# Kernel optimization log

Measured on AMD Instinct MI355X. Metric: run time of the kernel, lower is better.

Reference implementation:

```python
import jax, jax.numpy as jnp
import numpy as np

N_NODES = 50000
N_EDGES = 800000
N_GRAPHS = 128
F_IN = 36
HEADS1 = 10
OUT_DIM = 128


def _gat_layer(x, src, dst, W, a_src, a_dst, b, heads, out_c):
    # x: [N, Fin]; W: [Fin, heads*out_c]; a_src/a_dst: [heads, out_c]; b: [heads*out_c]
    N = x.shape[0]
    h = (x @ W).reshape(N, heads, out_c)                      # [N,H,C]
    al_s = jnp.einsum('nhc,hc->nh', h, a_src)                 # [N,H]
    al_d = jnp.einsum('nhc,hc->nh', h, a_dst)                 # [N,H]
    e = jax.nn.leaky_relu(al_s[src] + al_d[dst], negative_slope=0.2)  # [E,H]
    # segment-softmax over incoming edges of each dst node
    m = jax.ops.segment_max(e, dst, num_segments=N)
    m = jnp.where(jnp.isfinite(m), m, 0.0)
    p = jnp.exp(e - m[dst])
    s = jax.ops.segment_sum(p, dst, num_segments=N)
    alpha = p / (s[dst] + 1e-16)                              # [E,H]
    out = jax.ops.segment_sum(alpha[:, :, None] * h[src], dst, num_segments=N)  # [N,H,C]
    return out.reshape(N, heads * out_c) + b


def setup_inputs() -> dict:
    key = jax.random.key(0)
    ks = jax.random.split(key, 12)
    x = jax.random.normal(ks[0], (N_NODES, F_IN), dtype=jnp.float32)
    edge_index = jax.random.randint(ks[1], (2, N_EDGES), 0, N_NODES, dtype=jnp.int64)
    batch = jnp.sort(jax.random.randint(ks[2], (N_NODES,), 0, N_GRAPHS, dtype=jnp.int64))
    g = 0.1  # glorot-ish scale
    W1 = jax.random.normal(ks[3], (F_IN, HEADS1 * F_IN), dtype=jnp.float32) * g
    att_src1 = jax.random.normal(ks[4], (HEADS1, F_IN), dtype=jnp.float32) * g
    att_dst1 = jax.random.normal(ks[5], (HEADS1, F_IN), dtype=jnp.float32) * g
    b1 = jnp.zeros((HEADS1 * F_IN,), dtype=jnp.float32)
    W2 = jax.random.normal(ks[6], (HEADS1 * F_IN, OUT_DIM), dtype=jnp.float32) * g
    att_src2 = jax.random.normal(ks[7], (1, OUT_DIM), dtype=jnp.float32) * g
    att_dst2 = jax.random.normal(ks[8], (1, OUT_DIM), dtype=jnp.float32) * g
    b2 = jnp.zeros((OUT_DIM,), dtype=jnp.float32)
    fc_w = jax.random.normal(ks[9], (OUT_DIM, OUT_DIM), dtype=jnp.float32) * g
    fc_b = jnp.zeros((OUT_DIM,), dtype=jnp.float32)
    return {"x": x, "edge_index": edge_index, "batch": batch,
            "W1": W1, "att_src1": att_src1, "att_dst1": att_dst1, "b1": b1,
            "W2": W2, "att_src2": att_src2, "att_dst2": att_dst2, "b2": b2,
            "fc_w": fc_w, "fc_b": fc_b}


def reference(x, edge_index, batch, W1, att_src1, att_dst1, b1,
              W2, att_src2, att_dst2, b2, fc_w, fc_b):
    N = x.shape[0]
    # PyG GATConv adds self loops by default
    loops = jnp.arange(N, dtype=edge_index.dtype)
    src = jnp.concatenate([edge_index[0], loops])
    dst = jnp.concatenate([edge_index[1], loops])
    # eval mode: dropouts are identity
    h = jax.nn.elu(_gat_layer(x, src, dst, W1, att_src1, att_dst1, b1, HEADS1, F_IN))
    h = _gat_layer(h, src, dst, W2, att_src2, att_dst2, b2, 1, OUT_DIM)
    h = jax.nn.relu(h)
    # global max pool over graphs
    g = jax.ops.segment_max(h, batch, num_segments=N_GRAPHS)
    g = jnp.where(jnp.isfinite(g), g, 0.0)
    out = jax.nn.relu(g @ fc_w + fc_b)
    return out
```

## Files before the change

### kernel.cpp

```cpp
#include <hip/hip_runtime.h>
#include <hip/hip_fp16.h>
#include <math.h>

#define N_NODES  50000
#define N_EDGES  800000
#define E_TOT    850000
#define N_GRAPHS 128
#define F_IN     36
#define NH1      10
#define C1       36
#define D1       360
#define D2       128
#define XW       18

#define SCHUNK  512
#define NCHUNK  98

typedef unsigned int u32;

#if defined(__has_builtin)
#if __has_builtin(__builtin_amdgcn_fdot2)
#define HAVE_FDOT2 1
#endif
#endif
#ifndef HAVE_FDOT2
#define HAVE_FDOT2 0
#endif

typedef _Float16 h2v __attribute__((ext_vector_type(2)));

static __device__ __forceinline__ float2 h2f(u32 u) {
  __half2 h = __builtin_bit_cast(__half2, u);
  return __half22float2(h);
}
static __device__ __forceinline__ u32 f2h2(float a, float b) {
  __half2 h = __floats2half2_rn(a, b);
  return __builtin_bit_cast(u32, h);
}
static __device__ __forceinline__ float dot2acc(u32 a, u32 b, float acc) {
#if HAVE_FDOT2
  return __builtin_amdgcn_fdot2(__builtin_bit_cast(h2v, a), __builtin_bit_cast(h2v, b), acc, false);
#else
  float2 fa = h2f(a), fb = h2f(b);
  return fmaf(fa.x, fb.x, fmaf(fa.y, fb.y, acc));
#endif
}

__global__ void k_init(int* counts, u32* pool) {
  int i = blockIdx.x * blockDim.x + threadIdx.x;
  if (i < N_NODES) counts[i] = 0;
  if (i < N_GRAPHS * D2) pool[i] = 0u;
}

__global__ void k_hist(const int* ei, int* counts) {
  int e = blockIdx.x * blockDim.x + threadIdx.x;
  if (e >= E_TOT) return;
  int d = (e < N_EDGES) ? ei[N_EDGES + e] : (e - N_EDGES);
  atomicAdd(&counts[d], 1);
}

__global__ void k_scan1(const int* counts, int* partial) {
  __shared__ int red[256];
  int b = blockIdx.x, t = threadIdx.x;
  int base = b * SCHUNK;
  int v = 0;
  int i0 = base + t, i1 = base + t + 256;
  if (i0 < N_NODES) v += counts[i0];
  if (i1 < N_NODES) v += counts[i1];
  red[t] = v; __syncthreads();
  for (int off = 128; off; off >>= 1) {
    if (t < off) red[t] += red[t + off];
    __syncthreads();
  }
  if (t == 0) partial[b] = red[0];
}

__global__ void k_scan2(const int* partial, int* chunk_off, int* row_ptr) {
  if (threadIdx.x == 0 && blockIdx.x == 0) {
    int acc = 0;
    for (int i = 0; i < NCHUNK; i++) { chunk_off[i] = acc; acc += partial[i]; }
    row_ptr[N_NODES] = acc;
  }
}

__global__ void k_scan3(const int* counts, const int* chunk_off, int* row_ptr, int* nxt) {
  __shared__ int tmp[SCHUNK];
  int b = blockIdx.x, t = threadIdx.x;
  int i = b * SCHUNK + t;
  int v = (i < N_NODES) ? counts[i] : 0;
  tmp[t] = v; __syncthreads();
  for (int off = 1; off < SCHUNK; off <<= 1) {
    int x = (t >= off) ? tmp[t - off] : 0;
    __syncthreads();
    tmp[t] += x;
    __syncthreads();
  }
  if (i < N_NODES) {
    int excl = chunk_off[b] + tmp[t] - v;
    row_ptr[i] = excl;
    nxt[i] = excl;
  }
}

__global__ void k_scatter(const int* ei, int* nxt, int* csr_src) {
  int e = blockIdx.x * blockDim.x + threadIdx.x;
  if (e >= E_TOT) return;
  int s, d;
  if (e < N_EDGES) { s = ei[e]; d = ei[N_EDGES + e]; }
  else             { s = d = e - N_EDGES; }
  int pos = atomicAdd(&nxt[d], 1);
  csr_src[pos] = s;
}

__global__ void k_prep(const float* __restrict__ W1, const float* __restrict__ asrc,
                       const float* __restrict__ adst, const float* __restrict__ W2,
                       float* w_als, float* w_ald, u32* W1t2, u32* W2h) {
  int id = blockIdx.x * blockDim.x + threadIdx.x;
  if (id < D1) {
    int h = id / F_IN, k = id - h * F_IN;
    float sa = 0.f, sd = 0.f;
    for (int c = 0; c < C1; c++) {
      float wv = W1[k * D1 + h * C1 + c];
      sa = fmaf(wv, asrc[h * C1 + c], sa);
      sd = fmaf(wv, adst[h * C1 + c], sd);
    }
    w_als[id] = sa; w_ald[id] = sd;
  } else if (id < D1 + D1 * (F_IN / 2)) {
    int i = id - D1;
    int hc = i / (F_IN / 2), kp = i - hc * (F_IN / 2);
    W1t2[i] = f2h2(W1[(2 * kp) * D1 + hc], W1[(2 * kp + 1) * D1 + hc]);
  } else if (id < D1 + D1 * (F_IN / 2) + (D1 / 2) * D2) {
    int i = id - D1 - D1 * (F_IN / 2);
    int kp = i / D2, col = i - kp * D2;
    W2h[i] = f2h2(W2[(2 * kp) * D2 + col], W2[(2 * kp + 1) * D2 + col]);
  }
}

__global__ __launch_bounds__(256)
void k_als1(const float* __restrict__ x, const float* __restrict__ w_als,
            const float* __restrict__ w_ald, float* als, float* ald,
            u32* __restrict__ xh2) {
  __shared__ float xs[64][F_IN + 1];
  __shared__ float wa[D1], wd[D1];
  int t = threadIdx.x;
  int nb = blockIdx.x * 64;
  for (int i = t; i < D1; i += 256) { wa[i] = w_als[i]; wd[i] = w_ald[i]; }
  int lim = min(64, N_NODES - nb);
  for (int i = t; i < lim * F_IN; i += 256) {
    int n = i / F_IN, k = i - n * F_IN;
    xs[n][k] = x[(size_t)(nb + n) * F_IN + k];
  }
  __syncthreads();
  for (int i = t; i < lim * XW; i += 256) {
    int n = i / XW, kp = i - n * XW;
    xh2[(size_t)(nb + n) * XW + kp] = f2h2(xs[n][2 * kp], xs[n][2 * kp + 1]);
  }
  for (int pair = t; pair < lim * NH1; pair += 256) {
    int n = pair / NH1, h = pair - n * NH1;
    const float* xp = xs[n];
    const float* wap = &wa[h * F_IN];
    const float* wdp = &wd[h * F_IN];
    float sa = 0.f, sd = 0.f;
#pragma unroll
    for (int k = 0; k < F_IN; k++) {
      float xv = xp[k];
      sa = fmaf(xv, wap[k], sa);
      sd = fmaf(xv, wdp[k], sd);
    }
    als[(size_t)(nb + n) * NH1 + h] = sa;
    ald[(size_t)(nb + n) * NH1 + h] = sd;
  }
}

__global__ __launch_bounds__(256)
void k_agg1(const u32* __restrict__ xrow, const float* __restrict__ als,
            const float* __restrict__ ald, const int* __restrict__ row_ptr,
            const int* __restrict__ csr_src, u32* __restrict__ aggx2) {
  __shared__ float pl[4][64][NH1];
  int w = threadIdx.x >> 6, lane = threadIdx.x & 63;
  int node = blockIdx.x * 4 + w;
  int beg = row_ptr[node], end = row_ptr[node + 1];

  int h0 = lane / XW,  kp0 = lane - XW * h0;
  int s1 = lane + 64;
  int h1i = s1 / XW,   kp1 = s1 - XW * h1i;
  bool v2 = lane < 52;
  int s2 = v2 ? lane + 128 : 179;
  int h2i = s2 / XW,   kp2 = s2 - XW * h2i;

  float aldn[NH1];
#pragma unroll
  for (int h = 0; h < NH1; h++) aldn[h] = ald[(size_t)node * NH1 + h];
  float a0x = 0.f, a0y = 0.f, a1x = 0.f, a1y = 0.f, a2x = 0.f, a2y = 0.f;
  float sp[NH1];
#pragma unroll
  for (int h = 0; h < NH1; h++) sp[h] = 0.f;

  for (int base = beg; base < end; base += 64) {
    int cnt = min(64, end - base);
    float p[NH1];
    int msrc = 0;
    if (lane < cnt) {
      msrc = csr_src[base + lane];
      const float2* ap = (const float2*)(als + (size_t)msrc * NH1);
#pragma unroll
      for (int q = 0; q < 5; q++) {
        float2 v = ap[q];
        float v0 = v.x + aldn[2 * q];
        float v1 = v.y + aldn[2 * q + 1];
        v0 = v0 > 0.f ? v0 : 0.2f * v0;
        v1 = v1 > 0.f ? v1 : 0.2f * v1;
        p[2 * q] = __expf(v0);
        p[2 * q + 1] = __expf(v1);
      }
    } else {
#pragma unroll
      for (int h = 0; h < NH1; h++) p[h] = 0.f;
    }
#pragma unroll
    for (int h = 0; h < NH1; h++) sp[h] += p[h];
    float2* plw = (float2*)pl[w][lane];
#pragma unroll
    for (int q = 0; q < 5; q++) plw[q] = float2{p[2 * q], p[2 * q + 1]};
    __builtin_amdgcn_wave_barrier();

    int j2 = 0;
    for (; j2 + 2 <= cnt; j2 += 2) {
      int sA = __shfl(msrc, j2), sB = __shfl(msrc, j2 + 1);
      const u32* ra = xrow + (size_t)sA * XW;
      const u32* rb = xrow + (size_t)sB * XW;
      u32 ua0 = ra[kp0], ua1 = ra[kp1], ua2 = ra[kp2];
      u32 ub0 = rb[kp0], ub1 = rb[kp1], ub2 = rb[kp2];
      const float* pA = pl[w][j2];
      const float* pB = pl[w][j2 + 1];
      float cA0 = pA[h0], cA1 = pA[h1i], cA2 = pA[h2i];
      float cB0 = pB[h0], cB1 = pB[h1i], cB2 = pB[h2i];
      float2 f;
      f = h2f(ua0); a0x = fmaf(cA0, f.x, a0x); a0y = fmaf(cA0, f.y, a0y);
      f = h2f(ua1); a1x = fmaf(cA1, f.x, a1x); a1y = fmaf(cA1, f.y, a1y);
      f = h2f(ua2); a2x = fmaf(cA2, f.x, a2x); a2y = fmaf(cA2, f.y, a2y);
      f = h2f(ub0); a0x = fmaf(cB0, f.x, a0x); a0y = fmaf(cB0, f.y, a0y);
      f = h2f(ub1); a1x = fmaf(cB1, f.x, a1x); a1y = fmaf(cB1, f.y, a1y);
      f = h2f(ub2); a2x = fmaf(cB2, f.x, a2x); a2y = fmaf(cB2, f.y, a2y);
    }
    if (j2 < cnt) {
      int sA = __shfl(msrc, j2);
      const u32* ra = xrow + (size_t)sA * XW;
      u32 ua0 = ra[kp0], ua1 = ra[kp1], ua2 = ra[kp2];
      const float* pA = pl[w][j2];
      float cA0 = pA[h0], cA1 = pA[h1i], cA2 = pA[h2i];
      float2 f;
      f = h2f(ua0); a0x = fmaf(cA0, f.x, a0x); a0y = fmaf(cA0, f.y, a0y);
      f = h2f(ua1); a1x = fmaf(cA1, f.x, a1x); a1y = fmaf(cA1, f.y, a1y);
      f = h2f(ua2); a2x = fmaf(cA2, f.x, a2x); a2y = fmaf(cA2, f.y, a2y);
    }
    __builtin_amdgcn_wave_barrier();
  }

#pragma unroll
  for (int h = 0; h < NH1; h++) {
    float t = sp[h];
#pragma unroll
    for (int off = 32; off; off >>= 1) t += __shfl_xor(t, off);
    sp[h] = t;
  }
  float i0 = 1.f / (sp[h0] + 1e-16f);
  float i1 = 1.f / (sp[h1i] + 1e-16f);
  float i2 = 1.f / (sp[h2i] + 1e-16f);
  u32* orow = aggx2 + (size_t)node * (D1 / 2);
  orow[lane] = f2h2(a0x * i0, a0y * i0);
  orow[lane + 64] = f2h2(a1x * i1, a1y * i1);
  if (v2) orow[lane + 128] = f2h2(a2x * i2, a2y * i2);
}

#define MIX_NPB 32
__global__ __launch_bounds__(384)
void k_mix1(const u32* __restrict__ aggx2, const u32* __restrict__ W1t2,
            const float* __restrict__ b1, __half* __restrict__ hact) {
  __shared__ u32 ag[MIX_NPB][D1 / 2 + 4];
  int t = threadIdx.x;
  int nb = blockIdx.x * MIX_NPB;
  int lim = min(MIX_NPB, N_NODES - nb);
  const u32* gsrc = aggx2 + (size_t)nb * (D1 / 2);
  for (int i = t; i < lim * (D1 / 2); i += 384) {
    int n = i / (D1 / 2), k = i - n * (D1 / 2);
    ag[n][k] = gsrc[i];
  }
  __syncthreads();
  if (t < D1) {
    int h = t / C1;
    u32 wreg[F_IN / 2];
#pragma unroll
    for (int kp = 0; kp < F_IN / 2; kp++) wreg[kp] = W1t2[t * (F_IN / 2) + kp];
    float bj = b1[t];
    for (int n = 0; n < lim; n++) {
      const u32* a = &ag[n][h * (F_IN / 2)];
      float acc2 = 0.f;
#pragma unroll
      for (int kp = 0; kp < F_IN / 2; kp++) acc2 = dot2acc(a[kp], wreg[kp], acc2);
      float val = acc2 + bj;
      val = val > 0.f ? val : __expf(val) - 1.f;
      hact[(size_t)(nb + n) * D1 + t] = __float2half(val);
    }
  }
}

#define G2_NPB 16
__global__ __launch_bounds__(256)
void k_gemm2(const __half* __restrict__ hacth, const u32* __restrict__ W2h,
             __half* __restrict__ h2h) {
  __shared__ u32 hs2[D1 / 2][G2_NPB];
  int nb = blockIdx.x * G2_NPB;
  int t = threadIdx.x;
  for (int i = t; i < G2_NPB * (D1 / 2); i += 256) {
    int n = i / (D1 / 2), kp = i - n * (D1 / 2);
    hs2[kp][n] = ((const u32*)(hacth + (size_t)(nb + n) * D1))[kp];
  }
  __syncthreads();
  int col = t & 127, ng = t >> 7;
  float acc[8];
#pragma unroll
  for (int i = 0; i < 8; i++) acc[i] = 0.f;
#pragma unroll 2
  for (int kp = 0; kp < D1 / 2; kp++) {
    u32 wv = W2h[kp * D2 + col];
    uint4 r0 = *(const uint4*)&hs2[kp][ng * 8];
    uint4 r1 = *(const uint4*)&hs2[kp][ng * 8 + 4];
    acc[0] = dot2acc(r0.x, wv, acc[0]);
    acc[1] = dot2acc(r0.y, wv, acc[1]);
    acc[2] = dot2acc(r0.z, wv, acc[2]);
    acc[3] = dot2acc(r0.w, wv, acc[3]);
    acc[4] = dot2acc(r1.x, wv, acc[4]);
    acc[5] = dot2acc(r1.y, wv, acc[5]);
    acc[6] = dot2acc(r1.z, wv, acc[6]);
    acc[7] = dot2acc(r1.w, wv, acc[7]);
  }
#pragma unroll
  for (int i = 0; i < 8; i++)
    h2h[(size_t)(nb + ng * 8 + i) * D2 + col] = __float2half(acc[i]);
}

__global__ void k_als2(const __half* __restrict__ h2h, const float* __restrict__ asrc,
                       const float* __restrict__ adst, float* als, float* ald) {
  int node = blockIdx.x * 4 + (threadIdx.x >> 6);
  int lane = threadIdx.x & 63;
  const u32* hr = (const u32*)(h2h + (size_t)node * D2);
  float2 f = h2f(hr[lane]);
  float2 a = ((const float2*)asrc)[lane];
  float2 d = ((const float2*)adst)[lane];
  float ps = f.x * a.x + f.y * a.y;
  float pd = f.x * d.x + f.y * d.y;
#pragma unroll
  for (int off = 32; off; off >>= 1) { ps += __shfl_xor(ps, off); pd += __shfl_xor(pd, off); }
  if (lane == 0) { als[node] = ps; ald[node] = pd; }
}

__global__ __launch_bounds__(256)
void k_agg2(const __half* __restrict__ h2h, const float* __restrict__ als,
            const float* __restrict__ ald, const int* __restrict__ row_ptr,
            const int* __restrict__ csr_src, const float* __restrict__ b2,
            const int* __restrict__ batch, u32* __restrict__ pool) {
  int w = threadIdx.x >> 6, lane = threadIdx.x & 63;
  int node = blockIdx.x * 4 + w;
  int beg = row_ptr[node], end = row_ptr[node + 1];
  float aldn = ald[node];
  float ax = 0.f, ay = 0.f, ssum = 0.f;
  for (int base = beg; base < end; base += 64) {
    int cnt = min(64, end - base);
    int msrc = 0; float p = 0.f;
    if (lane < cnt) {
      msrc = csr_src[base + lane];
      float vv = als[msrc] + aldn;
      vv = vv > 0.f ? vv : 0.2f * vv;
      p = __expf(vv);
    }
    ssum += p;
    int j2 = 0;
    for (; j2 + 2 <= cnt; j2 += 2) {
      int sA = __shfl(msrc, j2), sB = __shfl(msrc, j2 + 1);
      float cA = __shfl(p, j2), cB = __shfl(p, j2 + 1);
      u32 ua = ((const u32*)(h2h + (size_t)sA * D2))[lane];
      u32 ub = ((const u32*)(h2h + (size_t)sB * D2))[lane];
      float2 f = h2f(ua); ax = fmaf(cA, f.x, ax); ay = fmaf(cA, f.y, ay);
      f = h2f(ub); ax = fmaf(cB, f.x, ax); ay = fmaf(cB, f.y, ay);
    }
    if (j2 < cnt) {
      int sA = __shfl(msrc, j2);
      float cA = __shfl(p, j2);
      u32 ua = ((const u32*)(h2h + (size_t)sA * D2))[lane];
      float2 f = h2f(ua); ax = fmaf(cA, f.x, ax); ay = fmaf(cA, f.y, ay);
    }
  }
  float t2 = ssum;
#pragma unroll
  for (int off = 32; off; off >>= 1) t2 += __shfl_xor(t2, off);
  float inv = 1.f / (t2 + 1e-16f);
  float2 bv = ((const float2*)b2)[lane];
  float vx = fmaxf(ax * inv + bv.x, 0.f);
  float vy = fmaxf(ay * inv + bv.y, 0.f);
  int g = batch[node];
  atomicMax(&pool[g * D2 + 2 * lane], __float_as_uint(vx));
  atomicMax(&pool[g * D2 + 2 * lane + 1], __float_as_uint(vy));
}

__global__ void k_final(const float* __restrict__ pool, const float* __restrict__ fcw,
                        const float* __restrict__ fcb, float* __restrict__ out) {
  __shared__ float ps[D2];
  int g = blockIdx.x, j = threadIdx.x;
  ps[j] = pool[g * D2 + j];
  __syncthreads();
  float acc = 0.f;
  for (int c = 0; c < D2; c++) acc = fmaf(ps[c], fcw[c * D2 + j], acc);
  acc += fcb[j];
  out[g * D2 + j] = acc > 0.f ? acc : 0.f;
}

extern "C" void kernel_launch(void* const* d_in, const int* in_sizes, int n_in,
                              void* d_out, int out_size, void* d_ws, size_t ws_size,
                              hipStream_t stream) {
  const float* x     = (const float*)d_in[0];
  const int*   ei    = (const int*)d_in[1];
  const int*   batch = (const int*)d_in[2];
  const float* W1    = (const float*)d_in[3];
  const float* asrc1 = (const float*)d_in[4];
  const float* adst1 = (const float*)d_in[5];
  const float* b1    = (const float*)d_in[6];
  const float* W2    = (const float*)d_in[7];
  const float* asrc2 = (const float*)d_in[8];
  const float* adst2 = (const float*)d_in[9];
  const float* b2    = (const float*)d_in[10];
  const float* fcw   = (const float*)d_in[11];
  const float* fcb   = (const float*)d_in[12];
  float* out = (float*)d_out;

  char* w = (char*)d_ws;
  size_t off = 0;
  auto alloc = [&](size_t bytes) -> char* {
    char* p = w + off;
    off = (off + bytes + 255) & ~(size_t)255;
    return p;
  };
  int* counts    = (int*)alloc((size_t)N_NODES * 4);
  int* row_ptr   = (int*)alloc((size_t)(N_NODES + 1) * 4);
  int* nxt       = (int*)alloc((size_t)N_NODES * 4);
  int* csr_src   = (int*)alloc((size_t)E_TOT * 4);
  int* partial   = (int*)alloc(NCHUNK * 4);
  int* chunk_off = (int*)alloc(NCHUNK * 4);
  float* als1    = (float*)alloc((size_t)N_NODES * NH1 * 4);
  float* ald1    = (float*)alloc((size_t)N_NODES * NH1 * 4);
  float* als2    = (float*)alloc((size_t)N_NODES * 4);
  float* ald2    = (float*)alloc((size_t)N_NODES * 4);
  u32*   pool    = (u32*)alloc((size_t)N_GRAPHS * D2 * 4);
  float* w_als   = (float*)alloc((size_t)D1 * 4);
  float* w_ald   = (float*)alloc((size_t)D1 * 4);
  u32*   W1t2    = (u32*)alloc((size_t)D1 * (F_IN / 2) * 4);
  u32*   W2h     = (u32*)alloc((size_t)(D1 / 2) * D2 * 4);
  u32*   xh2     = (u32*)alloc((size_t)N_NODES * XW * 4);
  u32*   aggx2   = (u32*)alloc((size_t)N_NODES * (D1 / 2) * 4);
  __half* hacth  = (__half*)alloc((size_t)N_NODES * D1 * 2);
  __half* h2h    = (__half*)alloc((size_t)N_NODES * D2 * 2);

  k_init<<<dim3(196), dim3(256), 0, stream>>>(counts, pool);
  k_hist<<<dim3((E_TOT + 255) / 256), dim3(256), 0, stream>>>(ei, counts);
  k_scan1<<<dim3(NCHUNK), dim3(256), 0, stream>>>(counts, partial);
  k_scan2<<<dim3(1), dim3(64), 0, stream>>>(partial, chunk_off, row_ptr);
  k_scan3<<<dim3(NCHUNK), dim3(SCHUNK), 0, stream>>>(counts, chunk_off, row_ptr, nxt);
  k_scatter<<<dim3((E_TOT + 255) / 256), dim3(256), 0, stream>>>(ei, nxt, csr_src);
  k_prep<<<dim3(117), dim3(256), 0, stream>>>(W1, asrc1, adst1, W2, w_als, w_ald, W1t2, W2h);

  k_als1<<<dim3((N_NODES + 63) / 64), dim3(256), 0, stream>>>(x, w_als, w_ald, als1, ald1, xh2);
  k_agg1<<<dim3(N_NODES / 4), dim3(256), 0, stream>>>(xh2, als1, ald1, row_ptr, csr_src, aggx2);
  k_mix1<<<dim3((N_NODES + MIX_NPB - 1) / MIX_NPB), dim3(384), 0, stream>>>(aggx2, W1t2, b1, hacth);

  k_gemm2<<<dim3(N_NODES / G2_NPB), dim3(256), 0, stream>>>(hacth, W2h, h2h);
  k_als2<<<dim3(N_NODES / 4), dim3(256), 0, stream>>>(h2h, asrc2, adst2, als2, ald2);
  k_agg2<<<dim3(N_NODES / 4), dim3(256), 0, stream>>>(h2h, als2, ald2, row_ptr, csr_src,
                                                      b2, batch, pool);

  k_final<<<dim3(N_GRAPHS), dim3(D2), 0, stream>>>((const float*)pool, fcw, fcb, out);

  (void)in_sizes; (void)n_in; (void)out_size; (void)ws_size;
}
```

Baseline: 481.2 us.

## Vectorize layer-2 gather with 16-byte loads across edge sub-groups, unroll layer-1 gather

The layer-2 aggregation now splits each wave into four 16-lane groups. Each group processes a different edge and loads a full 128-half row with uint4 loads. Partial sums are combined with cross-group shuffles, and the pool atomicMax is skipped when the existing value is already larger. Layer 1's gather loop is unrolled from 2 to 4 edges to raise memory-level parallelism. The changes trade more registers and shuffle reductions for fewer, wider loads and fewer atomics.

```diff
diff --git a/kernel.cpp b/kernel.cpp
--- a/kernel.cpp
+++ b/kernel.cpp
@@ -225,16 +225,25 @@
     __builtin_amdgcn_wave_barrier();
 
     int j2 = 0;
-    for (; j2 + 2 <= cnt; j2 += 2) {
-      int sA = __shfl(msrc, j2), sB = __shfl(msrc, j2 + 1);
+    for (; j2 + 4 <= cnt; j2 += 4) {
+      int sA = __shfl(msrc, j2),     sB = __shfl(msrc, j2 + 1);
+      int sC = __shfl(msrc, j2 + 2), sD = __shfl(msrc, j2 + 3);
       const u32* ra = xrow + (size_t)sA * XW;
       const u32* rb = xrow + (size_t)sB * XW;
+      const u32* rc = xrow + (size_t)sC * XW;
+      const u32* rd = xrow + (size_t)sD * XW;
       u32 ua0 = ra[kp0], ua1 = ra[kp1], ua2 = ra[kp2];
       u32 ub0 = rb[kp0], ub1 = rb[kp1], ub2 = rb[kp2];
+      u32 uc0 = rc[kp0], uc1 = rc[kp1], uc2 = rc[kp2];
+      u32 ud0 = rd[kp0], ud1 = rd[kp1], ud2 = rd[kp2];
       const float* pA = pl[w][j2];
       const float* pB = pl[w][j2 + 1];
+      const float* pC = pl[w][j2 + 2];
+      const float* pD = pl[w][j2 + 3];
       float cA0 = pA[h0], cA1 = pA[h1i], cA2 = pA[h2i];
       float cB0 = pB[h0], cB1 = pB[h1i], cB2 = pB[h2i];
+      float cC0 = pC[h0], cC1 = pC[h1i], cC2 = pC[h2i];
+      float cD0 = pD[h0], cD1 = pD[h1i], cD2 = pD[h2i];
       float2 f;
       f = h2f(ua0); a0x = fmaf(cA0, f.x, a0x); a0y = fmaf(cA0, f.y, a0y);
       f = h2f(ua1); a1x = fmaf(cA1, f.x, a1x); a1y = fmaf(cA1, f.y, a1y);
@@ -242,8 +251,14 @@
       f = h2f(ub0); a0x = fmaf(cB0, f.x, a0x); a0y = fmaf(cB0, f.y, a0y);
       f = h2f(ub1); a1x = fmaf(cB1, f.x, a1x); a1y = fmaf(cB1, f.y, a1y);
       f = h2f(ub2); a2x = fmaf(cB2, f.x, a2x); a2y = fmaf(cB2, f.y, a2y);
-    }
-    if (j2 < cnt) {
+      f = h2f(uc0); a0x = fmaf(cC0, f.x, a0x); a0y = fmaf(cC0, f.y, a0y);
+      f = h2f(uc1); a1x = fmaf(cC1, f.x, a1x); a1y = fmaf(cC1, f.y, a1y);
+      f = h2f(uc2); a2x = fmaf(cC2, f.x, a2x); a2y = fmaf(cC2, f.y, a2y);
+      f = h2f(ud0); a0x = fmaf(cD0, f.x, a0x); a0y = fmaf(cD0, f.y, a0y);
+      f = h2f(ud1); a1x = fmaf(cD1, f.x, a1x); a1y = fmaf(cD1, f.y, a1y);
+      f = h2f(ud2); a2x = fmaf(cD2, f.x, a2x); a2y = fmaf(cD2, f.y, a2y);
+    }
+    for (; j2 < cnt; j2++) {
       int sA = __shfl(msrc, j2);
       const u32* ra = xrow + (size_t)sA * XW;
       u32 ua0 = ra[kp0], ua1 = ra[kp1], ua2 = ra[kp2];
@@ -364,7 +379,13 @@
   int node = blockIdx.x * 4 + w;
   int beg = row_ptr[node], end = row_ptr[node + 1];
   float aldn = ald[node];
-  float ax = 0.f, ay = 0.f, ssum = 0.f;
+  int sub = lane >> 4;
+  int cq  = lane & 15;
+  float acc[8];
+#pragma unroll
+  for (int i = 0; i < 8; i++) acc[i] = 0.f;
+  float ssum = 0.f;
+
   for (int base = beg; base < end; base += 64) {
     int cnt = min(64, end - base);
     int msrc = 0; float p = 0.f;
@@ -375,32 +396,58 @@
       p = __expf(vv);
     }
     ssum += p;
-    int j2 = 0;
-    for (; j2 + 2 <= cnt; j2 += 2) {
-      int sA = __shfl(msrc, j2), sB = __shfl(msrc, j2 + 1);
-      float cA = __shfl(p, j2), cB = __shfl(p, j2 + 1);
-      u32 ua = ((const u32*)(h2h + (size_t)sA * D2))[lane];
-      u32 ub = ((const u32*)(h2h + (size_t)sB * D2))[lane];
-      float2 f = h2f(ua); ax = fmaf(cA, f.x, ax); ay = fmaf(cA, f.y, ay);
-      f = h2f(ub); ax = fmaf(cB, f.x, ax); ay = fmaf(cB, f.y, ay);
-    }
-    if (j2 < cnt) {
-      int sA = __shfl(msrc, j2);
-      float cA = __shfl(p, j2);
-      u32 ua = ((const u32*)(h2h + (size_t)sA * D2))[lane];
-      float2 f = h2f(ua); ax = fmaf(cA, f.x, ax); ay = fmaf(cA, f.y, ay);
-    }
+
+    int j4 = 0;
+    for (; j4 + 8 <= cnt; j4 += 8) {
+      int eA = j4 + sub, eB = j4 + 4 + sub;
+      int sA = __shfl(msrc, eA), sB = __shfl(msrc, eB);
+      float cA = __shfl(p, eA),  cB = __shfl(p, eB);
+      uint4 va = ((const uint4*)(h2h + (size_t)sA * D2))[cq];
+      uint4 vb = ((const uint4*)(h2h + (size_t)sB * D2))[cq];
+      float2 f;
+      f = h2f(va.x); acc[0] = fmaf(cA, f.x, acc[0]); acc[1] = fmaf(cA, f.y, acc[1]);
+      f = h2f(va.y); acc[2] = fmaf(cA, f.x, acc[2]); acc[3] = fmaf(cA, f.y, acc[3]);
+      f = h2f(va.z); acc[4] = fmaf(cA, f.x, acc[4]); acc[5] = fmaf(cA, f.y, acc[5]);
+      f = h2f(va.w); acc[6] = fmaf(cA, f.x, acc[6]); acc[7] = fmaf(cA, f.y, acc[7]);
+      f = h2f(vb.x); acc[0] = fmaf(cB, f.x, acc[0]); acc[1] = fmaf(cB, f.y, acc[1]);
+      f = h2f(vb.y); acc[2] = fmaf(cB, f.x, acc[2]); acc[3] = fmaf(cB, f.y, acc[3]);
+      f = h2f(vb.z); acc[4] = fmaf(cB, f.x, acc[4]); acc[5] = fmaf(cB, f.y, acc[5]);
+      f = h2f(vb.w); acc[6] = fmaf(cB, f.x, acc[6]); acc[7] = fmaf(cB, f.y, acc[7]);
+    }
+    for (; j4 < cnt; j4 += 4) {
+      int eA = j4 + sub;
+      int sA = __shfl(msrc, eA);
+      float cA = __shfl(p, eA);
+      uint4 va = ((const uint4*)(h2h + (size_t)sA * D2))[cq];
+      float2 f;
+      f = h2f(va.x); acc[0] = fmaf(cA, f.x, acc[0]); acc[1] = fmaf(cA, f.y, acc[1]);
+      f = h2f(va.y); acc[2] = fmaf(cA, f.x, acc[2]); acc[3] = fmaf(cA, f.y, acc[3]);
+      f = h2f(va.z); acc[4] = fmaf(cA, f.x, acc[4]); acc[5] = fmaf(cA, f.y, acc[5]);
+      f = h2f(va.w); acc[6] = fmaf(cA, f.x, acc[6]); acc[7] = fmaf(cA, f.y, acc[7]);
+    }
+  }
+
+#pragma unroll
+  for (int j = 0; j < 8; j++) {
+    acc[j] += __shfl_xor(acc[j], 16);
+    acc[j] += __shfl_xor(acc[j], 32);
   }
   float t2 = ssum;
 #pragma unroll
   for (int off = 32; off; off >>= 1) t2 += __shfl_xor(t2, off);
-  float inv = 1.f / (t2 + 1e-16f);
-  float2 bv = ((const float2*)b2)[lane];
-  float vx = fmaxf(ax * inv + bv.x, 0.f);
-  float vy = fmaxf(ay * inv + bv.y, 0.f);
-  int g = batch[node];
-  atomicMax(&pool[g * D2 + 2 * lane], __float_as_uint(vx));
-  atomicMax(&pool[g * D2 + 2 * lane + 1], __float_as_uint(vy));
+
+  if (sub == 0) {
+    float inv = 1.f / (t2 + 1e-16f);
+    int g = batch[node];
+    int cbase = 8 * cq;
+    u32* pbase = pool + (size_t)g * D2 + cbase;
+#pragma unroll
+    for (int j = 0; j < 8; j++) {
+      float v = fmaxf(acc[j] * inv + b2[cbase + j], 0.f);
+      u32 vb = __float_as_uint(v);
+      if (vb > pbase[j]) atomicMax(&pbase[j], vb);
+    }
+  }
 }
 
 __global__ void k_final(const float* __restrict__ pool, const float* __restrict__ fcw,
```

New measurement: 896.8 us. 1.86x slower.
